# Performance work log

Hardware: AMD Instinct MI355X
Metric: run time of the kernel (lower is better)

The kernel has to match this reference:

```python
import jax, jax.numpy as jnp
import numpy as np

N, E, F, H, G = 50000, 600000, 128, 128, 256
EPS = 1e-5
NEG_SLOPE = 0.2


def setup_inputs() -> dict:
    key = jax.random.key(0)
    ks = jax.random.split(key, 20)
    def w(k, shape, fan_in):
        return jax.random.normal(k, shape, jnp.float32) / np.sqrt(fan_in)
    x = jax.random.normal(ks[0], (N, F), jnp.float32)
    edge_index = jax.random.randint(ks[1], (2, E), 0, N, jnp.int32)
    batch = jnp.sort(jax.random.randint(ks[2], (N,), 0, G, jnp.int32))
    return {
        "x": x, "edge_index": edge_index, "batch": batch,
        "W1": w(ks[3], (F, H), F), "b1": jnp.zeros((H,), jnp.float32),
        "g1": jnp.ones((H,), jnp.float32), "be1": jnp.zeros((H,), jnp.float32),
        "Wg": w(ks[4], (H, H), H), "att_src": w(ks[5], (H,), H),
        "att_dst": w(ks[6], (H,), H), "bg": jnp.zeros((H,), jnp.float32),
        "g2": jnp.ones((H,), jnp.float32), "be2": jnp.zeros((H,), jnp.float32),
        "W3": w(ks[7], (H, H), H), "b3": jnp.zeros((H,), jnp.float32),
        "g3": jnp.ones((H,), jnp.float32), "be3": jnp.zeros((H,), jnp.float32),
        "fw1": w(ks[8], (H, H), H), "fb1": jnp.zeros((H,), jnp.float32),
        "fw2": w(ks[9], (H, 1), H), "fb2": jnp.zeros((1,), jnp.float32),
    }


def _with_self_loops(edge_index):
    loop = jnp.arange(N, dtype=edge_index.dtype)
    src = jnp.concatenate([edge_index[0], loop])
    dst = jnp.concatenate([edge_index[1], loop])
    return src, dst


def gcn_conv(x, W, b, src, dst):
    h = x @ W                                      # [N,H]
    deg = jax.ops.segment_sum(jnp.ones_like(dst, jnp.float32), dst, num_segments=N)
    dis = jnp.where(deg > 0, jax.lax.rsqrt(jnp.maximum(deg, 1.0)), 0.0)
    norm = dis[src] * dis[dst]                     # [E+N]
    msg = h[src] * norm[:, None]
    return jax.ops.segment_sum(msg, dst, num_segments=N) + b


def gat_conv(x, W, a_src, a_dst, b, src, dst):
    # single-head PyG GATConv with self loops
    h = x @ W                                      # [N,H]
    al_s = h @ a_src                               # [N]
    al_d = h @ a_dst
    e = jax.nn.leaky_relu(al_s[src] + al_d[dst], NEG_SLOPE)   # [E+N]
    m = jax.ops.segment_max(e, dst, num_segments=N)
    ex = jnp.exp(e - m[dst])
    denom = jax.ops.segment_sum(ex, dst, num_segments=N)
    alpha = ex / denom[dst]
    out = jax.ops.segment_sum(h[src] * alpha[:, None], dst, num_segments=N)
    return out + b


def batch_norm(x, gamma, beta):
    mu = jnp.mean(x, axis=0)
    var = jnp.var(x, axis=0)
    return gamma * (x - mu) * jax.lax.rsqrt(var + EPS) + beta


def reference(x, edge_index, batch, W1, b1, g1, be1, Wg, att_src, att_dst, bg,
              g2, be2, W3, b3, g3, be3, fw1, fb1, fw2, fb2):
    src, dst = _with_self_loops(edge_index)
    h = jax.nn.relu(batch_norm(gcn_conv(x, W1, b1, src, dst), g1, be1))
    # dropout = identity (eval mode)
    h = jax.nn.relu(batch_norm(gat_conv(h, Wg, att_src, att_dst, bg, src, dst), g2, be2))
    h = jax.nn.relu(batch_norm(gcn_conv(h, W3, b3, src, dst), g3, be3))
    # global mean pool over graphs
    sums = jax.ops.segment_sum(h, batch, num_segments=G)           # [G,H]
    cnts = jax.ops.segment_sum(jnp.ones((h.shape[0],), h.dtype), batch, num_segments=G)
    pooled = sums / jnp.maximum(cnts, 1.0)[:, None]
    z = jax.nn.relu(pooled @ fw1 + fb1)
    return z @ fw2 + fb2                                            # [G,1]
```

## Files before the change

kernel.cpp:

```cpp
#include <hip/hip_runtime.h>
#include <hip/hip_fp16.h>
#include <cstdint>

#define N_NODES 50000
#define N_EDGES 600000
#define HDIM    128
#define NGRAPH  256
#define EPSBN   1e-5f
#define NEG     0.2f
#define SCAN_B  196

__device__ __forceinline__ float lrelu(float v){ return v > 0.f ? v : NEG*v; }

typedef _Float16     f16x8 __attribute__((ext_vector_type(8)));
typedef float        f32x4 __attribute__((ext_vector_type(4)));
typedef unsigned int u32x4 __attribute__((ext_vector_type(4)));

__global__ void prep_kernel(const float* __restrict__ W1, const float* __restrict__ Wg,
                            const float* __restrict__ W3, __half* __restrict__ Wt1,
                            __half* __restrict__ Wtg, __half* __restrict__ Wt3,
                            const int* __restrict__ ei, int* __restrict__ degi,
                            const int* __restrict__ batch, int* __restrict__ start){
  int b = blockIdx.x;
  if (b < 192){
    const float* W = (b < 64) ? W1 : (b < 128 ? Wg : W3);
    __half*     Wt = (b < 64) ? Wt1 : (b < 128 ? Wtg : Wt3);
    int idx = (b & 63)*256 + threadIdx.x;
    int k = idx >> 7, n = idx & 127;
    int kc = k >> 5, q = (k >> 3) & 3, j = k & 7;
    int nt = n >> 4, c16 = n & 15;
    Wt[(((kc*8 + nt)*4 + q)*16 + c16)*8 + j] = __float2half(W[idx]);
  } else if (b < 192 + 2344){
    int e = (b - 192)*256 + threadIdx.x;
    if (e < N_EDGES) atomicAdd(&degi[ei[N_EDGES + e]], 1);
  } else {
    int i = (b - 192 - 2344)*256 + threadIdx.x;
    if (i >= N_NODES) return;
    int bb = batch[i];
    int p = (i == 0) ? -1 : batch[i-1];
    for (int g = p+1; g <= bb; ++g) start[g] = i;
    if (i == N_NODES-1)
      for (int g = bb+1; g <= NGRAPH; ++g) start[g] = N_NODES;
  }
}

__global__ void scan_kernel(const int* __restrict__ degi, int2* __restrict__ seg,
                            int* __restrict__ work, float* __restrict__ dis,
                            int* __restrict__ gctr){
  __shared__ int sm[256];
  __shared__ int base;
  int t = threadIdx.x; int i = blockIdx.x*256 + t;
  int v = (i < N_NODES) ? degi[i] : 0;
  if (i < N_NODES) dis[i] = rsqrtf((float)v + 1.f);
  sm[t] = v; __syncthreads();
  for (int off = 1; off < 256; off <<= 1){
    int add = (t >= off) ? sm[t - off] : 0;
    __syncthreads();
    sm[t] += add; __syncthreads();
  }
  if (t == 255) base = atomicAdd(gctr, sm[255]);
  __syncthreads();
  if (i < N_NODES){
    int r = base + sm[t] - v;
    seg[i] = make_int2(r, v);
    work[i] = r;
  }
}
__global__ void csr_scatter(const int* __restrict__ ei, int* __restrict__ work,
                            int* __restrict__ colx){
  int e = blockIdx.x*256 + threadIdx.x;
  if (e >= N_EDGES) return;
  int s = ei[e], d = ei[N_EDGES + e];
  int pos = atomicAdd(&work[d], 1);
  colx[pos] = s;
}

template<bool BN, bool F32IN, bool ATT, bool SCALE>
__global__ __launch_bounds__(256) void gemm_mfma(const void* __restrict__ Xv,
    const __half* __restrict__ Wt,
    const float* __restrict__ S, const float* __restrict__ Q,
    const float* __restrict__ gam, const float* __restrict__ bet,
    __half* __restrict__ Yh,
    const float* __restrict__ asr, const float* __restrict__ adt,
    float* __restrict__ al_s, float* __restrict__ al_d,
    const float* __restrict__ dis){
  __shared__ _Float16 scl[128], shl[128];
  const int t    = threadIdx.x;
  if (BN){
    if (t < 128){
      float mean = S[t] * (1.f/(float)N_NODES);
      float var  = fmaxf(Q[t]*(1.f/(float)N_NODES) - mean*mean, 0.f);
      float scale = gam[t]*rsqrtf(var + EPSBN);
      float shift = bet[t] - mean*scale;
      scl[t] = (_Float16)scale;
      shl[t] = (_Float16)shift;
    }
    __syncthreads();
  }
  const int wave = t >> 6, lane = t & 63;
  const int q    = lane >> 4, c16 = lane & 15;
  const int m0   = blockIdx.x*64 + wave*16;
  const int row  = m0 + c16;
  const int arow = (row > N_NODES-1) ? N_NODES-1 : row;

  f32x4 acc[8];
#pragma unroll
  for (int i = 0; i < 8; ++i) acc[i] = (f32x4){0.f,0.f,0.f,0.f};

  const f16x8* Wt8 = (const f16x8*)Wt;

#pragma unroll
  for (int kc = 0; kc < 4; ++kc){
    const int kof = kc*32 + q*8;
    f16x8 a;
    if (F32IN){
      const float* xp = (const float*)Xv + (long)arow*128 + kof;
      float4 x0 = *(const float4*)xp;
      float4 x1 = *(const float4*)(xp + 4);
      a[0]=(_Float16)x0.x; a[1]=(_Float16)x0.y; a[2]=(_Float16)x0.z; a[3]=(_Float16)x0.w;
      a[4]=(_Float16)x1.x; a[5]=(_Float16)x1.y; a[6]=(_Float16)x1.z; a[7]=(_Float16)x1.w;
    } else {
      f16x8 raw = *(const f16x8*)((const _Float16*)Xv + (long)arow*128 + kof);
      if (BN){
        f16x8 scv = *(const f16x8*)(scl + kof);
        f16x8 shv = *(const f16x8*)(shl + kof);
#pragma unroll
        for (int i = 0; i < 8; ++i){
          _Float16 v = (_Float16)(raw[i]*scv[i] + shv[i]);
          a[i] = v > (_Float16)0 ? v : (_Float16)0;
        }
      } else {
        a = raw;
      }
    }
#pragma unroll
    for (int nt = 0; nt < 8; ++nt){
      f16x8 b = Wt8[(kc*8 + nt)*64 + lane];
      acc[nt] = __builtin_amdgcn_mfma_f32_16x16x32_f16(b, a, acc[nt], 0, 0, 0);
    }
  }
  float rs = SCALE ? dis[arow] : 1.f;
  if (row < N_NODES){
    __half* yp = Yh + (long)row*128 + q*4;
#pragma unroll
    for (int nt = 0; nt < 8; ++nt){
      union { uint2 u; __half2 h[2]; } pk;
      pk.h[0] = __floats2half2_rn(acc[nt][0]*rs, acc[nt][1]*rs);
      pk.h[1] = __floats2half2_rn(acc[nt][2]*rs, acc[nt][3]*rs);
      *(uint2*)(yp + nt*16) = pk.u;
    }
  }
  if (ATT){
    float s = 0.f, d = 0.f;
#pragma unroll
    for (int nt = 0; nt < 8; ++nt){
      float4 av = *(const float4*)(asr + nt*16 + q*4);
      float4 bv = *(const float4*)(adt + nt*16 + q*4);
      s += acc[nt][0]*av.x + acc[nt][1]*av.y + acc[nt][2]*av.z + acc[nt][3]*av.w;
      d += acc[nt][0]*bv.x + acc[nt][1]*bv.y + acc[nt][2]*bv.z + acc[nt][3]*bv.w;
    }
    s += __shfl_xor(s, 16); s += __shfl_xor(s, 32);
    d += __shfl_xor(d, 16); d += __shfl_xor(d, 32);
    if (q == 0 && row < N_NODES){ al_s[row] = s; al_d[row] = d; }
  }
}

__global__ __launch_bounds__(256) void gcn_agg(const _Float16* __restrict__ Ah,
    const float* __restrict__ dis, const int2* __restrict__ seg,
    const int* __restrict__ colx, __half* __restrict__ Bh){
  const int t = threadIdx.x;
  const int grp = t >> 4, p = t & 15;
  const int n = blockIdx.x*16 + grp;
  const int2 sg = seg[n];
  const int e0 = sg.x, cnt = sg.y;
  f16x8 self = *(const f16x8*)(Ah + (long)n*128 + p*8);
  float acc[8];
#pragma unroll
  for (int i = 0; i < 8; ++i) acc[i] = (float)self[i];
  int j = 0;
  for (; j + 1 < cnt; j += 2){
    int s0 = colx[e0 + j];
    int s1 = colx[e0 + j + 1];
    f16x8 r0 = *(const f16x8*)(Ah + (long)s0*128 + p*8);
    f16x8 r1 = *(const f16x8*)(Ah + (long)s1*128 + p*8);
#pragma unroll
    for (int i = 0; i < 8; ++i) acc[i] += (float)r0[i] + (float)r1[i];
  }
  if (j < cnt){
    int s0 = colx[e0 + j];
    f16x8 r0 = *(const f16x8*)(Ah + (long)s0*128 + p*8);
#pragma unroll
    for (int i = 0; i < 8; ++i) acc[i] += (float)r0[i];
  }
  float dn = dis[n];
  union { u32x4 u; __half2 h[4]; } pk;
#pragma unroll
  for (int i = 0; i < 4; ++i)
    pk.h[i] = __floats2half2_rn(acc[2*i]*dn, acc[2*i+1]*dn);
  __builtin_nontemporal_store(pk.u, (u32x4*)(Bh + (long)n*128 + p*8));
}

__global__ __launch_bounds__(256) void gat_agg(const _Float16* __restrict__ Ah,
    const float* __restrict__ al_s, const float* __restrict__ al_d,
    const int2* __restrict__ seg, const int* __restrict__ colx,
    __half* __restrict__ Bh){
  const int t = threadIdx.x;
  const int grp = t >> 4, p = t & 15;
  const int n = blockIdx.x*16 + grp;
  const int2 sg = seg[n];
  const int e0 = sg.x, cnt = sg.y;
  const float adn = al_d[n];
  float m = lrelu(al_s[n] + adn);
  float denom = 1.f;
  f16x8 self = *(const f16x8*)(Ah + (long)n*128 + p*8);
  float acc[8];
#pragma unroll
  for (int i = 0; i < 8; ++i) acc[i] = (float)self[i];
  int j = 0;
  for (; j + 1 < cnt; j += 2){
    int s0 = colx[e0 + j];
    int s1 = colx[e0 + j + 1];
    float a0 = lrelu(al_s[s0] + adn);
    float a1 = lrelu(al_s[s1] + adn);
    f16x8 r0 = *(const f16x8*)(Ah + (long)s0*128 + p*8);
    f16x8 r1 = *(const f16x8*)(Ah + (long)s1*128 + p*8);
    float nm = fmaxf(m, fmaxf(a0, a1));
    float sc = __expf(m - nm);
    float w0 = __expf(a0 - nm);
    float w1 = __expf(a1 - nm);
    denom = denom*sc + w0 + w1;
    m = nm;
#pragma unroll
    for (int i = 0; i < 8; ++i)
      acc[i] = acc[i]*sc + w0*(float)r0[i] + w1*(float)r1[i];
  }
  if (j < cnt){
    int s0 = colx[e0 + j];
    float a0 = lrelu(al_s[s0] + adn);
    f16x8 r0 = *(const f16x8*)(Ah + (long)s0*128 + p*8);
    float nm = fmaxf(m, a0);
    float sc = __expf(m - nm);
    float w0 = __expf(a0 - nm);
    denom = denom*sc + w0;
#pragma unroll
    for (int i = 0; i < 8; ++i) acc[i] = acc[i]*sc + w0*(float)r0[i];
  }
  float rinv = 1.f / denom;
  union { u32x4 u; __half2 h[4]; } pk;
#pragma unroll
  for (int i = 0; i < 4; ++i)
    pk.h[i] = __floats2half2_rn(acc[2*i]*rinv, acc[2*i+1]*rinv);
  __builtin_nontemporal_store(pk.u, (u32x4*)(Bh + (long)n*128 + p*8));
}

__global__ void stats_h(const f16x8* __restrict__ X8,
                        float* __restrict__ S, float* __restrict__ Q){
  __shared__ float sb[16][16][8];
  __shared__ float qb[16][16][8];
  int t = threadIdx.x;
  int cg = t & 15, r = t >> 4;
  float s[8] = {0,0,0,0,0,0,0,0}, q[8] = {0,0,0,0,0,0,0,0};
  const int total = N_NODES*16;
  for (int idx = blockIdx.x*256 + t; idx < total; idx += gridDim.x*256){
    f16x8 v = X8[idx];
#pragma unroll
    for (int i = 0; i < 8; ++i){
      float f = (float)v[i];
      s[i] += f; q[i] += f*f;
    }
  }
#pragma unroll
  for (int i = 0; i < 8; ++i){ sb[r][cg][i] = s[i]; qb[r][cg][i] = q[i]; }
  __syncthreads();
  if (t < 128){
    int cg2 = t >> 3, j = t & 7;
    float as = 0.f, aq = 0.f;
#pragma unroll
    for (int r2 = 0; r2 < 16; ++r2){ as += sb[r2][cg2][j]; aq += qb[r2][cg2][j]; }
    atomicAdd(&S[cg2*8 + j], as);
    atomicAdd(&Q[cg2*8 + j], aq);
  }
}

__global__ void poolfinal(const __half* __restrict__ Bh, const int* __restrict__ start,
                          const float* __restrict__ S, const float* __restrict__ Q,
                          const float* __restrict__ gam, const float* __restrict__ bet,
                          const float* __restrict__ fw1, const float* __restrict__ fb1,
                          const float* __restrict__ fw2, const float* __restrict__ fb2,
                          float* __restrict__ out){
  __shared__ float scl[128], shl[128], psum[2][128], p[128], red[2];
  int t = threadIdx.x, gg = blockIdx.x;
  if (t < 128){
    float mean = S[t] * (1.f/(float)N_NODES);
    float var  = fmaxf(Q[t]*(1.f/(float)N_NODES) - mean*mean, 0.f);
    float scale = gam[t]*rsqrtf(var + EPSBN);
    scl[t] = scale;
    shl[t] = bet[t] - mean*scale;
  }
  __syncthreads();
  int s0 = start[gg], s1 = start[gg+1];
  int c = t & 127, h = t >> 7;
  float acc = 0.f;
  for (int n = s0 + h; n < s1; n += 2)
    acc += fmaxf(__half2float(Bh[(long)n*128 + c])*scl[c] + shl[c], 0.f);
  psum[h][c] = acc;
  __syncthreads();
  if (t < 128){
    float cnt = fmaxf((float)(s1 - s0), 1.f);
    p[t] = (psum[0][t] + psum[1][t]) / cnt;
  }
  __syncthreads();
  if (t < 128){
    float a = fb1[t];
    for (int k = 0; k < 128; ++k) a += p[k]*fw1[k*128 + t];
    float z = fmaxf(a, 0.f) * fw2[t];
    for (int off = 32; off; off >>= 1) z += __shfl_down(z, off);
    if ((t & 63) == 0) red[t >> 6] = z;
  }
  __syncthreads();
  if (t == 0) out[gg] = red[0] + red[1] + fb2[0];
}

extern "C" void kernel_launch(void* const* d_in, const int* in_sizes, int n_in,
                              void* d_out, int out_size, void* d_ws, size_t ws_size,
                              hipStream_t stream){
  const float* x    = (const float*)d_in[0];
  const int*   ei   = (const int*)d_in[1];
  const int*   batch= (const int*)d_in[2];
  const float* W1   = (const float*)d_in[3];
  const float* g1   = (const float*)d_in[5];
  const float* be1  = (const float*)d_in[6];
  const float* Wg   = (const float*)d_in[7];
  const float* asr  = (const float*)d_in[8];
  const float* adt  = (const float*)d_in[9];
  const float* g2   = (const float*)d_in[11];
  const float* be2  = (const float*)d_in[12];
  const float* W3   = (const float*)d_in[13];
  const float* g3   = (const float*)d_in[15];
  const float* be3  = (const float*)d_in[16];
  const float* fw1  = (const float*)d_in[17];
  const float* fb1  = (const float*)d_in[18];
  const float* fw2  = (const float*)d_in[19];
  const float* fb2  = (const float*)d_in[20];
  float* out = (float*)d_out;

  const long NH = (long)N_NODES*HDIM;
  __half* Ah    = (__half*)d_ws;
  __half* Bh    = Ah + NH;
  __half* Wt1   = Bh + NH;
  __half* Wtg   = Wt1 + 16384;
  __half* Wt3   = Wtg + 16384;
  float* dis    = (float*)(Wt3 + 16384);
  float* al_s   = dis + N_NODES;
  float* al_d   = al_s + N_NODES;
  int* deg_i    = (int*)(al_d + N_NODES);
  float* stats  = (float*)(deg_i + N_NODES);
  int* gctr     = (int*)(stats + 768);
  int2* seg     = (int2*)(gctr + 4);
  int* work     = (int*)(seg + N_NODES);
  int* colx     = work + N_NODES;
  int* start    = colx + N_EDGES;

  (void)hipMemsetAsync(deg_i, 0, (size_t)(N_NODES + 768 + 4) * sizeof(int), stream);

  const int TB = 256;
  const int gE  = (N_EDGES + TB - 1)/TB;
  const int gMM = (N_NODES + 63)/64;
  const int gAggG = N_NODES / 16;

  const _Float16* Ahf = (const _Float16*)Ah;
  const f16x8*    Bh8 = (const f16x8*)Bh;

  prep_kernel<<<192 + gE + SCAN_B, TB, 0, stream>>>(W1, Wg, W3, Wt1, Wtg, Wt3,
                                                    ei, deg_i, batch, start);
  scan_kernel<<<SCAN_B, TB, 0, stream>>>(deg_i, seg, work, dis, gctr);
  csr_scatter<<<gE, TB, 0, stream>>>(ei, work, colx);

  gemm_mfma<false,true,false,true><<<gMM, TB, 0, stream>>>(x, Wt1,
      nullptr, nullptr, nullptr, nullptr, Ah, nullptr, nullptr, nullptr, nullptr, dis);
  gcn_agg<<<gAggG, TB, 0, stream>>>(Ahf, dis, seg, colx, Bh);
  stats_h<<<512, TB, 0, stream>>>(Bh8, stats + 0, stats + 128);

  gemm_mfma<true,false,true,false><<<gMM, TB, 0, stream>>>(Bh, Wtg,
      stats + 0, stats + 128, g1, be1, Ah, asr, adt, al_s, al_d, nullptr);
  gat_agg<<<gAggG, TB, 0, stream>>>(Ahf, al_s, al_d, seg, colx, Bh);
  stats_h<<<512, TB, 0, stream>>>(Bh8, stats + 256, stats + 384);

  gemm_mfma<true,false,false,true><<<gMM, TB, 0, stream>>>(Bh, Wt3,
      stats + 256, stats + 384, g2, be2, Ah, nullptr, nullptr, nullptr, nullptr, dis);
  gcn_agg<<<gAggG, TB, 0, stream>>>(Ahf, dis, seg, colx, Bh);
  stats_h<<<512, TB, 0, stream>>>(Bh8, stats + 512, stats + 640);

  poolfinal<<<NGRAPH, TB, 0, stream>>>(Bh, start, stats + 512, stats + 640, g3, be3,
                                       fw1, fb1, fw2, fb2, out);
}
```

Before: 366.3 us.

## Sort nodes by degree bucket to balance aggregation wavefront work

```diff
diff --git a/kernel.cpp b/kernel.cpp
--- a/kernel.cpp
+++ b/kernel.cpp
@@ -46,12 +46,15 @@
 
 __global__ void scan_kernel(const int* __restrict__ degi, int2* __restrict__ seg,
                             int* __restrict__ work, float* __restrict__ dis,
-                            int* __restrict__ gctr){
+                            int* __restrict__ gctr, int* __restrict__ hist){
   __shared__ int sm[256];
   __shared__ int base;
   int t = threadIdx.x; int i = blockIdx.x*256 + t;
   int v = (i < N_NODES) ? degi[i] : 0;
-  if (i < N_NODES) dis[i] = rsqrtf((float)v + 1.f);
+  if (i < N_NODES){
+    dis[i] = rsqrtf((float)v + 1.f);
+    atomicAdd(&hist[min(v, 63)], 1);
+  }
   sm[t] = v; __syncthreads();
   for (int off = 1; off < 256; off <<= 1){
     int add = (t >= off) ? sm[t - off] : 0;
@@ -66,13 +69,33 @@
     work[i] = r;
   }
 }
+__global__ void hist_prefix(int* __restrict__ hist){
+  int t = threadIdx.x;
+  int v = hist[t];
+  int p = v;
+  for (int off = 1; off < 64; off <<= 1){
+    int u = __shfl_up(p, off);
+    if (t >= off) p += u;
+  }
+  hist[t] = p - v;
+}
 __global__ void csr_scatter(const int* __restrict__ ei, int* __restrict__ work,
-                            int* __restrict__ colx){
-  int e = blockIdx.x*256 + threadIdx.x;
-  if (e >= N_EDGES) return;
-  int s = ei[e], d = ei[N_EDGES + e];
-  int pos = atomicAdd(&work[d], 1);
-  colx[pos] = s;
+                            int* __restrict__ colx, const int2* __restrict__ seg,
+                            int* __restrict__ hist, int* __restrict__ order){
+  int b = blockIdx.x;
+  if (b < 2344){
+    int e = b*256 + threadIdx.x;
+    if (e >= N_EDGES) return;
+    int s = ei[e], d = ei[N_EDGES + e];
+    int pos = atomicAdd(&work[d], 1);
+    colx[pos] = s;
+  } else {
+    int i = (b - 2344)*256 + threadIdx.x;
+    if (i >= N_NODES) return;
+    int d = min(seg[i].y, 63);
+    int pos = atomicAdd(&hist[d], 1);
+    order[pos] = i;
+  }
 }
 
 template<bool BN, bool F32IN, bool ATT, bool SCALE>
@@ -167,10 +190,11 @@
 
 __global__ __launch_bounds__(256) void gcn_agg(const _Float16* __restrict__ Ah,
     const float* __restrict__ dis, const int2* __restrict__ seg,
-    const int* __restrict__ colx, __half* __restrict__ Bh){
+    const int* __restrict__ colx, const int* __restrict__ order,
+    __half* __restrict__ Bh){
   const int t = threadIdx.x;
   const int grp = t >> 4, p = t & 15;
-  const int n = blockIdx.x*16 + grp;
+  const int n = order[blockIdx.x*16 + grp];
   const int2 sg = seg[n];
   const int e0 = sg.x, cnt = sg.y;
   f16x8 self = *(const f16x8*)(Ah + (long)n*128 + p*8);
@@ -203,10 +227,10 @@
 __global__ __launch_bounds__(256) void gat_agg(const _Float16* __restrict__ Ah,
     const float* __restrict__ al_s, const float* __restrict__ al_d,
     const int2* __restrict__ seg, const int* __restrict__ colx,
-    __half* __restrict__ Bh){
+    const int* __restrict__ order, __half* __restrict__ Bh){
   const int t = threadIdx.x;
   const int grp = t >> 4, p = t & 15;
-  const int n = blockIdx.x*16 + grp;
+  const int n = order[blockIdx.x*16 + grp];
   const int2 sg = seg[n];
   const int e0 = sg.x, cnt = sg.y;
   const float adn = al_d[n];
@@ -356,12 +380,14 @@
   int* deg_i    = (int*)(al_d + N_NODES);
   float* stats  = (float*)(deg_i + N_NODES);
   int* gctr     = (int*)(stats + 768);
-  int2* seg     = (int2*)(gctr + 4);
+  int* hist     = gctr + 4;
+  int2* seg     = (int2*)(hist + 64);
   int* work     = (int*)(seg + N_NODES);
-  int* colx     = work + N_NODES;
+  int* order    = work + N_NODES;
+  int* colx     = order + N_NODES;
   int* start    = colx + N_EDGES;
 
-  (void)hipMemsetAsync(deg_i, 0, (size_t)(N_NODES + 768 + 4) * sizeof(int), stream);
+  (void)hipMemsetAsync(deg_i, 0, (size_t)(N_NODES + 768 + 4 + 64) * sizeof(int), stream);
 
   const int TB = 256;
   const int gE  = (N_EDGES + TB - 1)/TB;
@@ -373,22 +399,23 @@
 
   prep_kernel<<<192 + gE + SCAN_B, TB, 0, stream>>>(W1, Wg, W3, Wt1, Wtg, Wt3,
                                                     ei, deg_i, batch, start);
-  scan_kernel<<<SCAN_B, TB, 0, stream>>>(deg_i, seg, work, dis, gctr);
-  csr_scatter<<<gE, TB, 0, stream>>>(ei, work, colx);
+  scan_kernel<<<SCAN_B, TB, 0, stream>>>(deg_i, seg, work, dis, gctr, hist);
+  hist_prefix<<<1, 64, 0, stream>>>(hist);
+  csr_scatter<<<gE + SCAN_B, TB, 0, stream>>>(ei, work, colx, seg, hist, order);
 
   gemm_mfma<false,true,false,true><<<gMM, TB, 0, stream>>>(x, Wt1,
       nullptr, nullptr, nullptr, nullptr, Ah, nullptr, nullptr, nullptr, nullptr, dis);
-  gcn_agg<<<gAggG, TB, 0, stream>>>(Ahf, dis, seg, colx, Bh);
+  gcn_agg<<<gAggG, TB, 0, stream>>>(Ahf, dis, seg, colx, order, Bh);
   stats_h<<<512, TB, 0, stream>>>(Bh8, stats + 0, stats + 128);
 
   gemm_mfma<true,false,true,false><<<gMM, TB, 0, stream>>>(Bh, Wtg,
       stats + 0, stats + 128, g1, be1, Ah, asr, adt, al_s, al_d, nullptr);
-  gat_agg<<<gAggG, TB, 0, stream>>>(Ahf, al_s, al_d, seg, colx, Bh);
+  gat_agg<<<gAggG, TB, 0, stream>>>(Ahf, al_s, al_d, seg, colx, order, Bh);
   stats_h<<<512, TB, 0, stream>>>(Bh8, stats + 256, stats + 384);
 
   gemm_mfma<true,false,false,true><<<gMM, TB, 0, stream>>>(Bh, Wt3,
       stats + 256, stats + 384, g2, be2, Ah, nullptr, nullptr, nullptr, nullptr, dis);
-  gcn_agg<<<gAggG, TB, 0, stream>>>(Ahf, dis, seg, colx, Bh);
+  gcn_agg<<<gAggG, TB, 0, stream>>>(Ahf, dis, seg, colx, order, Bh);
   stats_h<<<512, TB, 0, stream>>>(Bh8, stats + 512, stats + 640);
 
   poolfinal<<<NGRAPH, TB, 0, stream>>>(Bh, start, stats + 512, stats + 640, g3, be3,
```

Measured after the change: 644.3 us. 1.76x slower.
